# Optimization experiments

Measured on AMD Instinct MI355X. Metric: run time of the kernel, lower is better.

The kernel has to match this reference:

```python
import jax, jax.numpy as jnp
import numpy as np


def _hardswish(x):
    return x * jnp.clip(x + 3.0, 0.0, 6.0) / 6.0


def _rel_coords_table(W):
    # [1, 2W-1, 2W-1, 2], log-spaced continuous relative coords (SwinV2)
    rc = jnp.arange(-(W - 1), W, dtype=jnp.float32)
    grid = jnp.stack(jnp.meshgrid(rc, rc, indexing='ij'), axis=-1)[None]
    grid = grid / float(W - 1) * 8.0
    return jnp.sign(grid) * jnp.log2(jnp.abs(grid) + 1.0) / np.float32(np.log2(8.0))


def _rel_pos_index(W):
    # [N, N] int indices into the (2W-1)^2 bias table
    coords = np.stack(np.meshgrid(np.arange(W), np.arange(W), indexing='ij')).reshape(2, -1)
    rel = (coords[:, :, None] - coords[:, None, :]).transpose(1, 2, 0)  # [N, N, 2]
    rel[:, :, 0] += W - 1
    rel[:, :, 1] += W - 1
    rel[:, :, 0] *= 2 * W - 1
    return jnp.asarray(rel.sum(-1))


def setup_inputs() -> dict:
    key = jax.random.key(0)
    ks = jax.random.split(key, 6)
    dim, num_heads, W = 512, 16, 8
    N = W * W
    B, nW = 2048, 64
    return {
        'x': jax.random.normal(ks[0], (B, N, dim), jnp.float32),
        'mask': jax.random.normal(ks[1], (nW, N, N), jnp.float32),
        'w_qkv': jax.random.normal(ks[2], (dim, 3 * dim), jnp.float32) * 0.02,
        'w_out': jax.random.normal(ks[3], (dim, dim), jnp.float32) * 0.02,
        'cpb_w1': jax.random.normal(ks[4], (2, 512), jnp.float32) * 0.02,
        'cpb_w2': jax.random.normal(ks[5], (512, num_heads), jnp.float32) * 0.02,
        'logits_scale': jnp.log(10.0 * jnp.ones((num_heads, 1, 1), jnp.float32)),
        'window_size': W,
        'num_heads': num_heads,
    }


def reference(x, mask, w_qkv, w_out, cpb_w1, cpb_w2, logits_scale, window_size, num_heads):
    B, N, C = x.shape
    hd = C // num_heads
    qkv = (x @ w_qkv).reshape(B, N, 3, num_heads, hd).transpose(2, 0, 3, 1, 4)
    q, k, v = qkv[0], qkv[1], qkv[2]  # [B, H, N, hd]

    # cosine attention (L2-normalized q, k) with clamped learned logit scale
    qn = q / jnp.clip(jnp.linalg.norm(q, axis=-1, keepdims=True), 1e-12)
    kn = k / jnp.clip(jnp.linalg.norm(k, axis=-1, keepdims=True), 1e-12)
    attn = jnp.einsum('bhnd,bhmd->bhnm', qn, kn)
    scale = jnp.exp(jnp.minimum(logits_scale, jnp.log(jnp.float32(100.0))))  # [H,1,1]
    attn = attn * scale[None]

    # continuous position bias via tiny MLP + index gather, sigmoid-scaled
    table = _rel_coords_table(window_size)                       # [1, 2W-1, 2W-1, 2]
    bias_table = (_hardswish(table @ cpb_w1) @ cpb_w2).reshape(-1, num_heads)
    idx = _rel_pos_index(window_size)                            # [N, N]
    bias = bias_table[idx.reshape(-1)].reshape(N, N, num_heads).transpose(2, 0, 1)
    attn = attn + 16.0 * jax.nn.sigmoid(bias)[None]

    if mask is not None:
        nW = mask.shape[0]
        attn = attn.reshape(B // nW, nW, num_heads, N, N) + mask[None, :, None]
        attn = attn.reshape(B, num_heads, N, N)

    # NOTE: original uses nn.Softmax(1) -> softmax over the HEAD axis; replicate faithfully
    attn = jax.nn.softmax(attn, axis=1)

    out = jnp.einsum('bhnm,bhmd->bhnd', attn, v).transpose(0, 2, 1, 3).reshape(B, N, C)
    return out @ w_out
```

## Files before the change

### kernel.cpp

```cpp
#include <hip/hip_runtime.h>
#include <hip/hip_bf16.h>

typedef unsigned short u16;
typedef unsigned int u32;
typedef __attribute__((ext_vector_type(8))) short bf16x8;
typedef __attribute__((ext_vector_type(4))) float f32x4;
typedef __attribute__((ext_vector_type(4))) float float4v;

__device__ __forceinline__ float bf2f(u16 v) {
  union { u32 u; float f; } x; x.u = ((u32)v) << 16; return x.f;
}
__device__ __forceinline__ u16 f2bf(float f) {
  union { u32 u; float f; } x; x.f = f;
  return (u16)((x.u + 0x7fffu + ((x.u >> 16) & 1u)) >> 16);
}

__device__ __forceinline__ void gload16(const void* g, void* l) {
  __builtin_amdgcn_global_load_lds(
      (const __attribute__((address_space(1))) u32*)g,
      (__attribute__((address_space(3))) u32*)l, 16, 0, 0);
}

#define MFMA16(a, bfr, cacc) __builtin_amdgcn_mfma_f32_16x16x32_bf16((a), (bfr), (cacc), 0, 0, 0)


__global__ void convert_bf16_kernel(const float* __restrict__ in,
                                    u16* __restrict__ out, int n8) {
  int t = blockIdx.x * blockDim.x + threadIdx.x;
  if (t >= n8) return;
  const float4v* p = (const float4v*)(in + (size_t)t * 8);
  float4v a = p[0], b = p[1];
  union { bf16x8 v; u16 s[8]; } o;
  o.s[0] = f2bf(a[0]); o.s[1] = f2bf(a[1]); o.s[2] = f2bf(a[2]); o.s[3] = f2bf(a[3]);
  o.s[4] = f2bf(b[0]); o.s[5] = f2bf(b[1]); o.s[6] = f2bf(b[2]); o.s[7] = f2bf(b[3]);
  *(bf16x8*)(out + (size_t)t * 8) = o.v;
}

__global__ void transpose_kernel(const float* __restrict__ in, u16* __restrict__ out,
                                 int R, int C) {
  int t = blockIdx.x * blockDim.x + threadIdx.x;
  if (t >= R * C) return;
  int c = t / R, r = t % R;
  out[t] = f2bf(in[r * C + c]);
}

__global__ void mask_t_kernel(const float* __restrict__ in, float* __restrict__ out) {
  int t = blockIdx.x * blockDim.x + threadIdx.x;
  if (t >= 64 * 4096) return;
  int wm = t >> 12, rest = t & 4095, m = rest >> 6, n = rest & 63;
  out[t] = in[wm * 4096 + n * 64 + m];
}

__global__ void bias_tab_kernel(const float* __restrict__ w1, const float* __restrict__ w2,
                                float* __restrict__ tab) {
  int t = blockIdx.x * blockDim.x + threadIdx.x;
  if (t >= 225 * 16) return;
  int r = t >> 4, h = t & 15;
  int i = r / 15, j = r % 15;
  float gi = (float)(i - 7) * (8.0f / 7.0f);
  float gj = (float)(j - 7) * (8.0f / 7.0f);
  float si = (gi > 0.f) ? 1.f : ((gi < 0.f) ? -1.f : 0.f);
  float sj = (gj > 0.f) ? 1.f : ((gj < 0.f) ? -1.f : 0.f);
  float t0 = si * log2f(fabsf(gi) + 1.0f) * (1.0f / 3.0f);
  float t1 = sj * log2f(fabsf(gj) + 1.0f) * (1.0f / 3.0f);
  float acc = 0.f;
  for (int k = 0; k < 512; ++k) {
    float a = t0 * w1[k] + t1 * w1[512 + k];
    float hs = a * fminf(fmaxf(a + 3.f, 0.f), 6.f) * (1.f / 6.f);
    acc += hs * w2[k * 16 + h];
  }
  tab[t] = acc;
}

__global__ void bias16_kernel(const float* __restrict__ tab, float* __restrict__ b16) {
  int t = blockIdx.x * blockDim.x + threadIdx.x;
  if (t >= 16 * 64 * 64) return;
  int h = t >> 12, nm = t & 4095, m = nm >> 6, n = nm & 63;
  int idx = ((n >> 3) - (m >> 3) + 7) * 15 + ((n & 7) - (m & 7) + 7);
  float b = tab[idx * 16 + h];
  b16[t] = 16.0f / (1.0f + expf(-b));
}

template <bool F32OUT>
__global__ __launch_bounds__(256) void gemm_bt(const u16* __restrict__ A,
                                               const u16* __restrict__ Bt,
                                               void* __restrict__ Cout,
                                               int M, int N, int K) {
  __shared__ u16 lA[128 * 64];
  __shared__ u16 lB[128 * 64];
  const int tid = threadIdx.x;
  const int w = tid >> 6, l = tid & 63;
  const int lg = l >> 4, li = l & 15;
  const int nbn = N >> 7;
  const int nwg = gridDim.x;
  int bidx = blockIdx.x;
  int q = nwg >> 3, r = nwg & 7;
  int xcd = bidx & 7, pos = bidx >> 3;
  int swz = (xcd < r ? xcd * (q + 1) : r * (q + 1) + (xcd - r) * q) + pos;
  int bm = swz / nbn, bn = swz % nbn;
  const int wr = w >> 1, wc = w & 1;

  f32x4 acc[4][4];
#pragma unroll
  for (int i = 0; i < 4; i++)
#pragma unroll
    for (int j = 0; j < 4; j++) acc[i][j] = (f32x4){0.f, 0.f, 0.f, 0.f};

  const u16* Abase = A + (size_t)(bm * 128) * K;
  const u16* Bbase = Bt + (size_t)(bn * 128) * K;

  for (int k0 = 0; k0 < K; k0 += 64) {
#pragma unroll
    for (int i = 0; i < 4; ++i) {
      int c = w * 256 + i * 64 + l;
      int row = c >> 3, kc = c & 7;
      int kcs = kc ^ (row & 7);
      gload16(Abase + (size_t)row * K + k0 + kcs * 8, (u16*)lA + c * 8);
      gload16(Bbase + (size_t)row * K + k0 + kcs * 8, (u16*)lB + c * 8);
    }
    __syncthreads();
#pragma unroll
    for (int kk = 0; kk < 2; ++kk) {
      bf16x8 af[4], bfr[4];
#pragma unroll
      for (int t = 0; t < 4; ++t) {
        int row = wr * 64 + t * 16 + li;
        af[t] = *(const bf16x8*)&lA[row * 64 + (((kk * 4 + lg) ^ (row & 7)) << 3)];
        int col = wc * 64 + t * 16 + li;
        bfr[t] = *(const bf16x8*)&lB[col * 64 + (((kk * 4 + lg) ^ (col & 7)) << 3)];
      }
#pragma unroll
      for (int tm = 0; tm < 4; ++tm)
#pragma unroll
        for (int tn = 0; tn < 4; ++tn)
          acc[tm][tn] = MFMA16(af[tm], bfr[tn], acc[tm][tn]);
    }
    __syncthreads();
  }
  int r0 = bm * 128 + wr * 64 + lg * 4;
  int c0 = bn * 128 + wc * 64 + li;
#pragma unroll
  for (int tm = 0; tm < 4; ++tm)
#pragma unroll
    for (int tn = 0; tn < 4; ++tn)
#pragma unroll
      for (int j = 0; j < 4; ++j) {
        size_t off = (size_t)(r0 + tm * 16 + j) * N + c0 + tn * 16;
        if (F32OUT)
          ((float*)Cout)[off] = acc[tm][tn][j];
        else
          ((u16*)Cout)[off] = f2bf(acc[tm][tn][j]);
      }
}

__global__ __launch_bounds__(256) void gemm_qk(const u16* __restrict__ A,
                                               const u16* __restrict__ Bt,
                                               u16* __restrict__ Cq,
                                               const float* __restrict__ lscale,
                                               int M, int K) {
  __shared__ u16 lds[128 * 136];
  u16* lA = lds;
  u16* lB = lds + 8192;
  const int tid = threadIdx.x;
  const int w = tid >> 6, l = tid & 63;
  const int lg = l >> 4, li = l & 15;
  const int nbn = 8;
  const int nwg = gridDim.x;
  int bidx = blockIdx.x;
  int q = nwg >> 3, r = nwg & 7;
  int xcd = bidx & 7, pos = bidx >> 3;
  int swz = (xcd < r ? xcd * (q + 1) : r * (q + 1) + (xcd - r) * q) + pos;
  int bm = swz / nbn, bn = swz % nbn;
  const int wr = w >> 1, wc = w & 1;

  f32x4 acc[4][4];
#pragma unroll
  for (int i = 0; i < 4; i++)
#pragma unroll
    for (int j = 0; j < 4; j++) acc[i][j] = (f32x4){0.f, 0.f, 0.f, 0.f};

  const u16* Abase = A + (size_t)(bm * 128) * K;
  const u16* Bbase = Bt + (size_t)(bn * 128) * K;

  for (int k0 = 0; k0 < K; k0 += 64) {
#pragma unroll
    for (int i = 0; i < 4; ++i) {
      int c = w * 256 + i * 64 + l;
      int row = c >> 3, kc = c & 7;
      int kcs = kc ^ (row & 7);
      gload16(Abase + (size_t)row * K + k0 + kcs * 8, lA + c * 8);
      gload16(Bbase + (size_t)row * K + k0 + kcs * 8, lB + c * 8);
    }
    __syncthreads();
#pragma unroll
    for (int kk = 0; kk < 2; ++kk) {
      bf16x8 af[4], bfr[4];
#pragma unroll
      for (int t = 0; t < 4; ++t) {
        int row = wr * 64 + t * 16 + li;
        af[t] = *(const bf16x8*)&lA[row * 64 + (((kk * 4 + lg) ^ (row & 7)) << 3)];
        int col = wc * 64 + t * 16 + li;
        bfr[t] = *(const bf16x8*)&lB[col * 64 + (((kk * 4 + lg) ^ (col & 7)) << 3)];
      }
#pragma unroll
      for (int tm = 0; tm < 4; ++tm)
#pragma unroll
        for (int tn = 0; tn < 4; ++tn)
          acc[tm][tn] = MFMA16(af[tm], bfr[tn], acc[tm][tn]);
    }
    __syncthreads();
  }

  const int s_t = bn >> 2;
  const int hq = (bn & 3) * 4;
  float scv[2];
  if (s_t == 0) {
    scv[0] = __expf(fminf(lscale[hq + wc * 2 + 0], 4.6051702f));
    scv[1] = __expf(fminf(lscale[hq + wc * 2 + 1], 4.6051702f));
  } else {
    scv[0] = scv[1] = 1.0f;
  }
#pragma unroll
  for (int tm = 0; tm < 4; ++tm)
#pragma unroll
    for (int g = 0; g < 2; ++g) {
      f32x4 s2;
#pragma unroll
      for (int j = 0; j < 4; ++j)
        s2[j] = acc[tm][2 * g][j] * acc[tm][2 * g][j] +
                acc[tm][2 * g + 1][j] * acc[tm][2 * g + 1][j];
#pragma unroll
      for (int m = 1; m <= 8; m <<= 1)
#pragma unroll
        for (int j = 0; j < 4; ++j) s2[j] += __shfl_xor(s2[j], m);
#pragma unroll
      for (int j = 0; j < 4; ++j) {
        float rn = scv[g] / fmaxf(sqrtf(s2[j]), 1e-12f);
        acc[tm][2 * g][j] *= rn;
        acc[tm][2 * g + 1][j] *= rn;
      }
    }
  u16* ct = lds;
#pragma unroll
  for (int tm = 0; tm < 4; ++tm)
#pragma unroll
    for (int tn = 0; tn < 4; ++tn)
#pragma unroll
      for (int j = 0; j < 4; ++j)
        ct[(wr * 64 + tm * 16 + lg * 4 + j) * 136 + wc * 64 + tn * 16 + li] =
            f2bf(acc[tm][tn][j]);
  __syncthreads();
  {
    int rr = tid >> 2;
    int c8 = (tid & 3) * 8;
#pragma unroll
    for (int bh = 0; bh < 2; ++bh)
#pragma unroll
      for (int ht = 0; ht < 4; ++ht) {
        bf16x8 v = *(const bf16x8*)(ct + (bh * 64 + rr) * 136 + ht * 32 + c8);
        size_t base = ((size_t)(s_t * 16 + hq + ht) * 2048 + (bm * 2 + bh)) * 2048;
        *(bf16x8*)(Cq + base + rr * 32 + c8) = v;
      }
  }
}

__global__ __launch_bounds__(256) void gemm_v(const u16* __restrict__ A,
                                              const u16* __restrict__ Bt,
                                              u16* __restrict__ Cq,
                                              int M, int K) {
  __shared__ u16 lds[128 * 136];
  u16* lA = lds;
  u16* lB = lds + 8192;
  const int tid = threadIdx.x;
  const int w = tid >> 6, l = tid & 63;
  const int lg = l >> 4, li = l & 15;
  const int nbn = 4;
  const int nwg = gridDim.x;
  int bidx = blockIdx.x;
  int q = nwg >> 3, r = nwg & 7;
  int xcd = bidx & 7, pos = bidx >> 3;
  int swz = (xcd < r ? xcd * (q + 1) : r * (q + 1) + (xcd - r) * q) + pos;
  int bm = swz / nbn, bn = swz % nbn;
  const int wr = w >> 1, wc = w & 1;

  f32x4 acc[4][4];
#pragma unroll
  for (int i = 0; i < 4; i++)
#pragma unroll
    for (int j = 0; j < 4; j++) acc[i][j] = (f32x4){0.f, 0.f, 0.f, 0.f};

  const u16* Abase = A + (size_t)(bm * 128) * K;
  const u16* Bbase = Bt + (size_t)(bn * 128) * K;

  for (int k0 = 0; k0 < K; k0 += 64) {
#pragma unroll
    for (int i = 0; i < 4; ++i) {
      int c = w * 256 + i * 64 + l;
      int row = c >> 3, kc = c & 7;
      int kcs = kc ^ (row & 7);
      gload16(Abase + (size_t)row * K + k0 + kcs * 8, lA + c * 8);
      gload16(Bbase + (size_t)row * K + k0 + kcs * 8, lB + c * 8);
    }
    __syncthreads();
#pragma unroll
    for (int kk = 0; kk < 2; ++kk) {
      bf16x8 af[4], bfr[4];
#pragma unroll
      for (int t = 0; t < 4; ++t) {
        int row = wr * 64 + t * 16 + li;
        af[t] = *(const bf16x8*)&lA[row * 64 + (((kk * 4 + lg) ^ (row & 7)) << 3)];
        int col = wc * 64 + t * 16 + li;
        bfr[t] = *(const bf16x8*)&lB[col * 64 + (((kk * 4 + lg) ^ (col & 7)) << 3)];
      }
#pragma unroll
      for (int tm = 0; tm < 4; ++tm)
#pragma unroll
        for (int tn = 0; tn < 4; ++tn)
          acc[tm][tn] = MFMA16(af[tm], bfr[tn], acc[tm][tn]);
    }
    __syncthreads();
  }

  const int hq = bn * 4;
  u16* ctT = lds;
#pragma unroll
  for (int tm = 0; tm < 4; ++tm)
#pragma unroll
    for (int tn = 0; tn < 4; ++tn)
#pragma unroll
      for (int j = 0; j < 4; ++j)
        ctT[(wc * 64 + tn * 16 + li) * 136 + wr * 64 + tm * 16 + lg * 4 + j] =
            f2bf(acc[tm][tn][j]);
  __syncthreads();
#pragma unroll
  for (int r2 = 0; r2 < 8; ++r2) {
    int id = r2 * 256 + tid;
    int colc = id >> 4;
    int seg = id & 15;
    bf16x8 v = *(const bf16x8*)&ctT[colc * 136 + seg * 8];
    int ht = colc >> 5, d = colc & 31;
    int wi = seg >> 3, n0 = (seg & 7) * 8;
    size_t base = ((size_t)(32 + hq + ht) * 2048 + (bm * 2 + wi)) * 2048;
    *(bf16x8*)(Cq + base + d * 64 + n0) = v;
  }
}

__global__ __launch_bounds__(512, 2) void attn2(const u16* __restrict__ qkv,
                                                const float* __restrict__ maskT,
                                                const float* __restrict__ bias16T,
                                                u16* __restrict__ aout) {
  __shared__ float S[16 * 1088];
  u16* P16 = (u16*)S;
  float* ob = S;
  const int tid = threadIdx.x;
  const int w = tid >> 6, l = tid & 63;
  const int lg = l >> 4, li = l & 15;
  const int b = blockIdx.x, wm = b & 63;
  const float* maskT_w = maskT + wm * 4096;

  bf16x8 qfr[2][4];
#pragma unroll
  for (int hp = 0; hp < 2; ++hp) {
    const u16* qb = qkv + ((size_t)(w + hp * 8) * 2048 + b) * 2048;
#pragma unroll
    for (int tn = 0; tn < 4; ++tn)
      qfr[hp][tn] = *(const bf16x8*)(qb + (tn * 16 + li) * 32 + lg * 8);
  }

  f32x4 oacc[2][4][2];
#pragma unroll
  for (int hp = 0; hp < 2; ++hp)
#pragma unroll
    for (int i = 0; i < 4; ++i) {
      oacc[hp][i][0] = (f32x4){0.f, 0.f, 0.f, 0.f};
      oacc[hp][i][1] = (f32x4){0.f, 0.f, 0.f, 0.f};
    }

#pragma unroll
  for (int c = 0; c < 4; ++c) {
#pragma unroll
    for (int hp = 0; hp < 2; ++hp) {
      int h = w + hp * 8;
      const u16* kb = qkv + ((size_t)(16 + h) * 2048 + b) * 2048;
      const float* biasT_h = bias16T + h * 4096;
      bf16x8 kfc = *(const bf16x8*)(kb + (c * 16 + li) * 32 + lg * 8);
      int mg = c * 16 + li;
#pragma unroll
      for (int tn = 0; tn < 4; ++tn) {
        f32x4 z = {0.f, 0.f, 0.f, 0.f};
        f32x4 s = MFMA16(qfr[hp][tn], kfc, z);
        float4v b4 = *(const float4v*)(biasT_h + mg * 64 + tn * 16 + lg * 4);
        float4v m4 = *(const float4v*)(maskT_w + mg * 64 + tn * 16 + lg * 4);
        *(float4v*)&S[h * 1088 + li * 68 + tn * 16 + lg * 4] = s + b4 + m4;
      }
    }
    __syncthreads();
#pragma unroll
    for (int pp = 0; pp < 2; ++pp) {
      int p = tid + pp * 512;
      int base = (p >> 6) * 68 + (p & 63);
      float vals[16];
      float mx = -3.0e38f;
#pragma unroll
      for (int hh = 0; hh < 16; ++hh) {
        vals[hh] = S[hh * 1088 + base];
        mx = fmaxf(mx, vals[hh]);
      }
      float sum = 0.f;
#pragma unroll
      for (int hh = 0; hh < 16; ++hh) {
        float e = __expf(vals[hh] - mx);
        vals[hh] = e;
        sum += e;
      }
      float inv = 1.0f / sum;
#pragma unroll
      for (int hh = 0; hh < 16; ++hh)
        P16[(hh * 1088 + base) * 2] = f2bf(vals[hh] * inv);
    }
    __syncthreads();
#pragma unroll
    for (int hp = 0; hp < 2; ++hp) {
      int h = w + hp * 8;
      const u16* vbT = qkv + ((size_t)(32 + h) * 2048 + b) * 2048;
      bf16x8 vf[2];
      if (lg < 2) {
#pragma unroll
        for (int td = 0; td < 2; ++td)
          vf[td] = *(const bf16x8*)(vbT + (td * 16 + li) * 64 + c * 16 + lg * 8);
      } else {
#pragma unroll
        for (int td = 0; td < 2; ++td)
#pragma unroll
          for (int e = 0; e < 8; ++e) vf[td][e] = 0;
      }
#pragma unroll
      for (int tn = 0; tn < 4; ++tn) {
        bf16x8 pf;
#pragma unroll
        for (int e = 0; e < 8; ++e)
          pf[e] = (lg < 2)
                      ? (short)P16[(h * 1088 + (lg * 8 + e) * 68 + tn * 16 + li) * 2]
                      : (short)0;
        oacc[hp][tn][0] = MFMA16(pf, vf[0], oacc[hp][tn][0]);
        oacc[hp][tn][1] = MFMA16(pf, vf[1], oacc[hp][tn][1]);
      }
    }
    __syncthreads();
  }

#pragma unroll
  for (int tn = 0; tn < 4; ++tn) {
#pragma unroll
    for (int hp = 0; hp < 2; ++hp) {
      int h = w + hp * 8;
#pragma unroll
      for (int td = 0; td < 2; ++td)
#pragma unroll
        for (int j = 0; j < 4; ++j)
          ob[(lg * 4 + j) * 516 + h * 32 + td * 16 + li] = oacc[hp][tn][td][j];
    }
    __syncthreads();
    {
      int rr = tid >> 5, c16 = (tid & 31) * 16;
      const float* src = ob + rr * 516 + c16;
      u16* dst = aout + ((size_t)b * 64 + tn * 16 + rr) * 512 + c16;
#pragma unroll
      for (int half = 0; half < 2; ++half) {
        union { bf16x8 v; u16 u[8]; } o;
#pragma unroll
        for (int e = 0; e < 8; ++e) o.u[e] = f2bf(src[half * 8 + e]);
        *(bf16x8*)(dst + half * 8) = o.v;
      }
    }
    __syncthreads();
  }
}

extern "C" void kernel_launch(void* const* d_in, const int* in_sizes, int n_in,
                              void* d_out, int out_size, void* d_ws, size_t ws_size,
                              hipStream_t stream) {
  const float* x = (const float*)d_in[0];
  const float* mask = (const float*)d_in[1];
  const float* w_qkv = (const float*)d_in[2];
  const float* w_out = (const float*)d_in[3];
  const float* cpb_w1 = (const float*)d_in[4];
  const float* cpb_w2 = (const float*)d_in[5];
  const float* lscale = (const float*)d_in[6];
  float* out = (float*)d_out;

  char* ws = (char*)d_ws;
  u16* wqkvT = (u16*)ws;
  u16* woutT = (u16*)(ws + 1572864ull);
  float* btab = (float*)(ws + 2097152ull);
  float* b16 = (float*)(ws + 2113536ull);
  float* maskT = (float*)(ws + 2375680ull);
  u16* qkv_ws = (u16*)(ws + 19152896ull);
  u16* xb = (u16*)(ws + 19152896ull + 402653184ull);
  u16* attn_out = xb;

  transpose_kernel<<<(512 * 1536 + 255) / 256, 256, 0, stream>>>(w_qkv, wqkvT, 512, 1536);
  transpose_kernel<<<(512 * 512 + 255) / 256, 256, 0, stream>>>(w_out, woutT, 512, 512);
  bias_tab_kernel<<<(225 * 16 + 255) / 256, 256, 0, stream>>>(cpb_w1, cpb_w2, btab);
  bias16_kernel<<<(16 * 64 * 64 + 255) / 256, 256, 0, stream>>>(btab, b16);
  mask_t_kernel<<<(64 * 4096 + 255) / 256, 256, 0, stream>>>(mask, maskT);

  convert_bf16_kernel<<<(131072 * 64 + 255) / 256, 256, 0, stream>>>(x, xb, 131072 * 64);

  gemm_qk<<<8192, 256, 0, stream>>>(xb, wqkvT, qkv_ws, lscale, 131072, 512);
  gemm_v<<<4096, 256, 0, stream>>>(xb, wqkvT + (size_t)1024 * 512, qkv_ws, 131072, 512);

  attn2<<<2048, 512, 0, stream>>>(qkv_ws, maskT, b16, attn_out);

  gemm_bt<true><<<4096, 256, 0, stream>>>(attn_out, woutT, out, 131072, 512, 512);
}
```

Measured before the change: 906.9 us.

## Halve attention chunk size to cut LDS use and raise occupancy

The attn2 kernel now processes the key dimension in 8 chunks of 8 columns instead of 4 chunks of 16. This halves the fp32 score buffer in shared memory and adds a separate, transposed bf16 probability buffer that is read with vector loads. Launch bounds go from 2 to 4 blocks per SM, with the chunk loop kept rolled, so more blocks can be resident. In exchange, half the lanes compute wasted MFMA work, there are more barriers per block, and V fragments are reloaded per tile.

```diff
diff --git a/kernel.cpp b/kernel.cpp
--- a/kernel.cpp
+++ b/kernel.cpp
@@ -4,6 +4,7 @@
 typedef unsigned short u16;
 typedef unsigned int u32;
 typedef __attribute__((ext_vector_type(8))) short bf16x8;
+typedef __attribute__((ext_vector_type(4))) short bf16x4;
 typedef __attribute__((ext_vector_type(4))) float f32x4;
 typedef __attribute__((ext_vector_type(4))) float float4v;
 
@@ -345,12 +346,12 @@
   }
 }
 
-__global__ __launch_bounds__(512, 2) void attn2(const u16* __restrict__ qkv,
+__global__ __launch_bounds__(512, 4) void attn2(const u16* __restrict__ qkv,
                                                 const float* __restrict__ maskT,
                                                 const float* __restrict__ bias16T,
                                                 u16* __restrict__ aout) {
-  __shared__ float S[16 * 1088];
-  u16* P16 = (u16*)S;
+  __shared__ float S[16 * 544];
+  __shared__ u16 P16r[16 * 768];
   float* ob = S;
   const int tid = threadIdx.x;
   const int w = tid >> 6, l = tid & 63;
@@ -376,34 +377,34 @@
       oacc[hp][i][1] = (f32x4){0.f, 0.f, 0.f, 0.f};
     }
 
-#pragma unroll
-  for (int c = 0; c < 4; ++c) {
+#pragma unroll 1
+  for (int c = 0; c < 8; ++c) {
 #pragma unroll
     for (int hp = 0; hp < 2; ++hp) {
       int h = w + hp * 8;
       const u16* kb = qkv + ((size_t)(16 + h) * 2048 + b) * 2048;
       const float* biasT_h = bias16T + h * 4096;
-      bf16x8 kfc = *(const bf16x8*)(kb + (c * 16 + li) * 32 + lg * 8);
-      int mg = c * 16 + li;
+      bf16x8 kfc = *(const bf16x8*)(kb + (c * 8 + (li & 7)) * 32 + lg * 8);
+      int mg = c * 8 + (li & 7);
 #pragma unroll
       for (int tn = 0; tn < 4; ++tn) {
         f32x4 z = {0.f, 0.f, 0.f, 0.f};
         f32x4 s = MFMA16(qfr[hp][tn], kfc, z);
-        float4v b4 = *(const float4v*)(biasT_h + mg * 64 + tn * 16 + lg * 4);
-        float4v m4 = *(const float4v*)(maskT_w + mg * 64 + tn * 16 + lg * 4);
-        *(float4v*)&S[h * 1088 + li * 68 + tn * 16 + lg * 4] = s + b4 + m4;
-      }
-    }
-    __syncthreads();
-#pragma unroll
-    for (int pp = 0; pp < 2; ++pp) {
-      int p = tid + pp * 512;
-      int base = (p >> 6) * 68 + (p & 63);
+        if (li < 8) {
+          float4v b4 = *(const float4v*)(biasT_h + mg * 64 + tn * 16 + lg * 4);
+          float4v m4 = *(const float4v*)(maskT_w + mg * 64 + tn * 16 + lg * 4);
+          *(float4v*)&S[h * 544 + li * 68 + tn * 16 + lg * 4] = s + b4 + m4;
+        }
+      }
+    }
+    __syncthreads();
+    {
+      int m = tid >> 6, n = tid & 63;
       float vals[16];
       float mx = -3.0e38f;
 #pragma unroll
       for (int hh = 0; hh < 16; ++hh) {
-        vals[hh] = S[hh * 1088 + base];
+        vals[hh] = S[hh * 544 + m * 68 + n];
         mx = fmaxf(mx, vals[hh]);
       }
       float sum = 0.f;
@@ -416,34 +417,38 @@
       float inv = 1.0f / sum;
 #pragma unroll
       for (int hh = 0; hh < 16; ++hh)
-        P16[(hh * 1088 + base) * 2] = f2bf(vals[hh] * inv);
+        P16r[hh * 768 + n * 12 + m] = f2bf(vals[hh] * inv);
     }
     __syncthreads();
 #pragma unroll
     for (int hp = 0; hp < 2; ++hp) {
       int h = w + hp * 8;
       const u16* vbT = qkv + ((size_t)(32 + h) * 2048 + b) * 2048;
-      bf16x8 vf[2];
-      if (lg < 2) {
-#pragma unroll
-        for (int td = 0; td < 2; ++td)
-          vf[td] = *(const bf16x8*)(vbT + (td * 16 + li) * 64 + c * 16 + lg * 8);
-      } else {
-#pragma unroll
-        for (int td = 0; td < 2; ++td)
-#pragma unroll
-          for (int e = 0; e < 8; ++e) vf[td][e] = 0;
+      bf16x8 vf;
+      if (lg == 0) {
       }
 #pragma unroll
       for (int tn = 0; tn < 4; ++tn) {
         bf16x8 pf;
-#pragma unroll
-        for (int e = 0; e < 8; ++e)
-          pf[e] = (lg < 2)
-                      ? (short)P16[(h * 1088 + (lg * 8 + e) * 68 + tn * 16 + li) * 2]
-                      : (short)0;
-        oacc[hp][tn][0] = MFMA16(pf, vf[0], oacc[hp][tn][0]);
-        oacc[hp][tn][1] = MFMA16(pf, vf[1], oacc[hp][tn][1]);
+        if (lg == 0) {
+          const u16* pb = P16r + h * 768 + (tn * 16 + li) * 12;
+          bf16x4 plo = *(const bf16x4*)pb;
+          bf16x4 phi = *(const bf16x4*)(pb + 4);
+          pf[0] = plo[0]; pf[1] = plo[1]; pf[2] = plo[2]; pf[3] = plo[3];
+          pf[4] = phi[0]; pf[5] = phi[1]; pf[6] = phi[2]; pf[7] = phi[3];
+        } else {
+#pragma unroll
+          for (int e = 0; e < 8; ++e) pf[e] = 0;
+        }
+#pragma unroll
+        for (int td = 0; td < 2; ++td) {
+          if (lg == 0)
+            vf = *(const bf16x8*)(vbT + (td * 16 + li) * 64 + c * 8);
+          else
+#pragma unroll
+            for (int e = 0; e < 8; ++e) vf[e] = 0;
+          oacc[hp][tn][td] = MFMA16(pf, vf, oacc[hp][tn][td]);
+        }
       }
     }
     __syncthreads();
```

Result: slower. 1.077 ms (+18.7%).
